# Kernel optimization log

Hardware: AMD Instinct MI355X
Metric: run time of the kernel (lower is better)

## Reference

```python
import jax, jax.numpy as jnp
import numpy as np

N_NODES = 50000

def setup_inputs() -> dict:
    key = jax.random.key(0)
    ks = jax.random.split(key, 8)
    d_in, d_h = 128, 128
    x = jax.random.normal(ks[0], (N_NODES, d_in), dtype=jnp.float32)
    edge_index = jax.random.randint(ks[1], (2, 800000), 0, N_NODES, dtype=jnp.int64)
    edge_pairs = jax.random.randint(ks[2], (1000000, 2), 0, N_NODES, dtype=jnp.int64)
    W_gcn = jax.random.normal(ks[3], (d_in, d_h), dtype=jnp.float32) / np.sqrt(d_in)
    b_gcn = jnp.zeros((d_h,), dtype=jnp.float32)
    W1 = jax.random.normal(ks[4], (2 * d_h, d_h), dtype=jnp.float32) / np.sqrt(2 * d_h)
    b1 = jnp.zeros((d_h,), dtype=jnp.float32)
    W2 = jax.random.normal(ks[5], (d_h, 1), dtype=jnp.float32) / np.sqrt(d_h)
    b2 = jnp.zeros((1,), dtype=jnp.float32)
    return {"x": x, "edge_index": edge_index, "edge_pairs": edge_pairs,
            "W_gcn": W_gcn, "b_gcn": b_gcn, "W1": W1, "b1": b1, "W2": W2, "b2": b2}

def gcn_conv(x, edge_index, W, b):
    # PyG GCNConv default: add self-loops, symmetric normalization.
    n = x.shape[0]
    loop = jnp.arange(n, dtype=edge_index.dtype)
    src = jnp.concatenate([edge_index[0], loop])  # [E+N]
    dst = jnp.concatenate([edge_index[1], loop])
    deg = jax.ops.segment_sum(jnp.ones(src.shape[0], dtype=x.dtype), dst, num_segments=n)
    dinv = jnp.where(deg > 0, jax.lax.rsqrt(deg), 0.0)
    norm = dinv[src] * dinv[dst]                  # [E+N]
    h = x @ W                                     # [N, H]
    agg = jax.ops.segment_sum(h[src] * norm[:, None], dst, num_segments=n)
    return agg + b

def reference(x, edge_index, edge_pairs, W_gcn, b_gcn, W1, b1, W2, b2):
    h = gcn_conv(x, edge_index, W_gcn, b_gcn)      # [N, H]
    e = jnp.concatenate([h[edge_pairs[:, 0]], h[edge_pairs[:, 1]]], axis=-1)  # [P, 2H]
    edge_logits = jax.nn.relu(e @ W1 + b1) @ W2 + b2  # [P, 1]
    return edge_logits, edge_pairs, h
```

## Files before the change

kernel.cpp:

```cpp
#include <hip/hip_runtime.h>
#include <hip/hip_fp16.h>

#define WG 256

typedef _Float16 f16;
typedef _Float16 hv2 __attribute__((ext_vector_type(2)));
typedef _Float16 f16x4 __attribute__((ext_vector_type(4)));
typedef _Float16 f16x8 __attribute__((ext_vector_type(8)));
typedef float f32x4 __attribute__((ext_vector_type(4)));

__global__ __launch_bounds__(WG) void k_count2(const int* __restrict__ dst,
                                               int* __restrict__ deg,
                                               int* __restrict__ rank,
                                               const int* __restrict__ pairs,
                                               int* __restrict__ pdeg,
                                               int* __restrict__ prank,
                                               int e, int p) {
    int i = blockIdx.x * WG + threadIdx.x;
    if (i < e) {
        rank[i] = atomicAdd(&deg[dst[i]], 1);
    } else if (i < e + p) {
        int j = i - e;
        prank[j] = atomicAdd(&pdeg[pairs[2 * j]], 1);
    }
}

__global__ __launch_bounds__(WG) void k_scan1x2(const int* __restrict__ deg,
                                                float* __restrict__ dinv,
                                                int* __restrict__ base,
                                                int* __restrict__ bsum,
                                                const int* __restrict__ pdeg,
                                                int* __restrict__ pbase,
                                                int* __restrict__ pbsum,
                                                int n, int nb) {
    __shared__ int t[WG];
    int tid = threadIdx.x;
    bool second = (blockIdx.x >= (unsigned)nb);
    int bid = second ? (blockIdx.x - nb) : blockIdx.x;
    const int* src = second ? pdeg : deg;
    int* dstb = second ? pbase : base;
    int* bs = second ? pbsum : bsum;
    int i = bid * WG + tid;
    int v = (i < n) ? src[i] : 0;
    if (!second && i < n) dinv[i] = rsqrtf((float)(v + 1));
    t[tid] = v;
    __syncthreads();
    for (int o = 1; o < WG; o <<= 1) {
        int add = (tid >= o) ? t[tid - o] : 0;
        __syncthreads();
        t[tid] += add;
        __syncthreads();
    }
    if (i < n) dstb[i] = t[tid] - v;
    if (tid == WG - 1) bs[bid] = t[WG - 1];
}

__global__ __launch_bounds__(WG) void k_scan23x2(int* __restrict__ base,
                                                 const int* __restrict__ bsum,
                                                 int* __restrict__ pbase,
                                                 const int* __restrict__ pbsum,
                                                 int n, int e, int p, int nb) {
    __shared__ int t[WG];
    int tid = threadIdx.x;
    bool second = (blockIdx.x >= (unsigned)nb);
    int bid = second ? (blockIdx.x - nb) : blockIdx.x;
    const int* bs = second ? pbsum : bsum;
    int* dstb = second ? pbase : base;
    int total = second ? p : e;
    int v = (tid < nb) ? bs[tid] : 0;
    t[tid] = v;
    __syncthreads();
    for (int o = 1; o < WG; o <<= 1) {
        int add = (tid >= o) ? t[tid - o] : 0;
        __syncthreads();
        t[tid] += add;
        __syncthreads();
    }
    int off = t[bid] - ((bid < nb) ? bs[bid] : 0);
    int i = bid * WG + tid;
    if (i < n) {
        dstb[i] += off;
        if (i == n - 1) dstb[n] = total;
    }
}

__global__ __launch_bounds__(WG) void k_fill2(const int* __restrict__ src,
                                              const int* __restrict__ dst,
                                              const int* __restrict__ base,
                                              const int* __restrict__ rank,
                                              int* __restrict__ esrc,
                                              const int* __restrict__ pairs,
                                              const int* __restrict__ pbase,
                                              const int* __restrict__ prank,
                                              int2* __restrict__ plist,
                                              int e, int p) {
    int i = blockIdx.x * WG + threadIdx.x;
    if (i < e) {
        esrc[base[dst[i]] + rank[i]] = src[i];
    } else if (i < e + p) {
        int j = i - e;
        int a = pairs[2 * j], b = pairs[2 * j + 1];
        plist[pbase[a] + prank[j]] = make_int2(b, j);
    }
}

__global__ __launch_bounds__(WG) void k_misc(const float* __restrict__ Wg,
                                             f16* __restrict__ Wgt,
                                             const float* __restrict__ W1,
                                             f16* __restrict__ W1t,
                                             const int* __restrict__ pairs,
                                             float* __restrict__ outp, int n4) {
    int b = blockIdx.x;
    if (b < 64) {
        int i = b * WG + threadIdx.x;
        int k = i & 127, nI = i >> 7;
        Wgt[i] = (f16)Wg[(size_t)k * 128 + nI];
    } else if (b < 192) {
        int i = (b - 64) * WG + threadIdx.x;
        int k = i & 255, nI = i >> 8;
        W1t[i] = (f16)W1[(size_t)k * 128 + nI];
    } else {
        int i = (b - 192) * WG + threadIdx.x;
        if (i < n4) {
            int4 v = ((const int4*)pairs)[i];
            ((float4*)outp)[i] = make_float4((float)v.x, (float)v.y, (float)v.z, (float)v.w);
        }
    }
}

__global__ __launch_bounds__(WG) void k_mm_hpk(const float* __restrict__ A,
                                               const f16* __restrict__ Wt,
                                               const float* __restrict__ dinv,
                                               __half2* __restrict__ Out, int n) {
    __shared__ f16 As[64][136];
    __shared__ f16 Bs[128][136];
    const int tid = threadIdx.x;
    const int row0 = blockIdx.x * 64;
    for (int f = tid; f < 128 * 16; f += WG) {
        int r = f >> 4, c = f & 15;
        *(float4*)&Bs[r][c * 8] = ((const float4*)Wt)[r * 16 + c];
    }
    for (int f = tid; f < 64 * 32; f += WG) {
        int r = f >> 5, c = f & 31;
        float4 v = make_float4(0.f, 0.f, 0.f, 0.f);
        if (row0 + r < n) v = ((const float4*)A)[(size_t)(row0 + r) * 32 + c];
        *(f16x4*)&As[r][c * 4] = (f16x4){(f16)v.x, (f16)v.y, (f16)v.z, (f16)v.w};
    }
    __syncthreads();
    const int wv = tid >> 6, lane = tid & 63, m = lane & 15, quad = lane >> 4;
    f32x4 acc[8];
#pragma unroll
    for (int t = 0; t < 8; ++t) acc[t] = (f32x4){0.f, 0.f, 0.f, 0.f};
#pragma unroll
    for (int kk = 0; kk < 4; ++kk) {
        f16x8 af = *(f16x8*)&As[wv * 16 + m][kk * 32 + quad * 8];
#pragma unroll
        for (int t = 0; t < 8; ++t) {
            f16x8 bf = *(f16x8*)&Bs[t * 16 + m][kk * 32 + quad * 8];
            acc[t] = __builtin_amdgcn_mfma_f32_16x16x32_f16(af, bf, acc[t], 0, 0, 0);
        }
    }
#pragma unroll
    for (int r = 0; r < 4; ++r) {
        int row = row0 + wv * 16 + quad * 4 + r;
        if (row < n) {
            float dv = dinv[row];
#pragma unroll
            for (int t = 0; t < 4; ++t)
                Out[(size_t)row * 64 + t * 16 + m] =
                    __floats2half2_rn(acc[t][r] * dv, acc[t + 4][r] * dv);
        }
    }
}

__global__ __launch_bounds__(WG) void k_mm_uv(const float* __restrict__ A,
                                              const f16* __restrict__ W1t,
                                              const float* __restrict__ b1,
                                              __half2* __restrict__ Up,
                                              __half2* __restrict__ Vp, int n) {
    __shared__ f16 As[64][136];
    __shared__ f16 Bs[128][136];
    const int tid = threadIdx.x;
    const int row0 = blockIdx.x * 64;
    for (int f = tid; f < 64 * 32; f += WG) {
        int r = f >> 5, c = f & 31;
        float4 v = make_float4(0.f, 0.f, 0.f, 0.f);
        if (row0 + r < n) v = ((const float4*)A)[(size_t)(row0 + r) * 32 + c];
        *(f16x4*)&As[r][c * 4] = (f16x4){(f16)v.x, (f16)v.y, (f16)v.z, (f16)v.w};
    }
    const int wv = tid >> 6, lane = tid & 63, m = lane & 15, quad = lane >> 4;
    f32x4 acc[8];
#pragma unroll
    for (int ph = 0; ph < 2; ++ph) {
        if (ph) __syncthreads();
        for (int f = tid; f < 128 * 16; f += WG) {
            int r = f >> 4, c = f & 15;
            *(float4*)&Bs[r][c * 8] = *(const float4*)(W1t + (size_t)r * 256 + ph * 128 + c * 8);
        }
        __syncthreads();
#pragma unroll
        for (int t = 0; t < 8; ++t) acc[t] = (f32x4){0.f, 0.f, 0.f, 0.f};
#pragma unroll
        for (int kk = 0; kk < 4; ++kk) {
            f16x8 af = *(f16x8*)&As[wv * 16 + m][kk * 32 + quad * 8];
#pragma unroll
            for (int t = 0; t < 8; ++t) {
                f16x8 bf = *(f16x8*)&Bs[t * 16 + m][kk * 32 + quad * 8];
                acc[t] = __builtin_amdgcn_mfma_f32_16x16x32_f16(af, bf, acc[t], 0, 0, 0);
            }
        }
        __half2* Out = ph ? Vp : Up;
#pragma unroll
        for (int t = 0; t < 4; ++t) {
            float bl = 0.f, bh = 0.f;
            if (!ph) { bl = b1[t * 16 + m]; bh = b1[t * 16 + m + 64]; }
#pragma unroll
            for (int r = 0; r < 4; ++r) {
                int row = row0 + wv * 16 + quad * 4 + r;
                if (row < n)
                    Out[(size_t)row * 64 + t * 16 + m] =
                        __floats2half2_rn(acc[t][r] + bl, acc[t + 4][r] + bh);
            }
        }
    }
}

__global__ __launch_bounds__(WG) void k_gather(const __half2* __restrict__ Hpk,
                                               const float* __restrict__ dinv,
                                               const float* __restrict__ bg,
                                               const int* __restrict__ base,
                                               const int* __restrict__ esrc,
                                               float* __restrict__ outh, int n) {
    int tid = threadIdx.x;
    int node = blockIdx.x * 16 + (tid >> 4);
    int sub = tid & 15;
    if (node >= n) return;
    int4 hh = *(const int4*)(Hpk + (size_t)node * 64 + 4 * sub);
    const int* hp = (const int*)&hh;
    float accl[4], acch[4];
#pragma unroll
    for (int k = 0; k < 4; ++k) {
        hv2 h = __builtin_bit_cast(hv2, hp[k]);
        accl[k] = (float)h[0];
        acch[k] = (float)h[1];
    }
    int j = base[node], jend = base[node + 1];
    for (; j + 4 <= jend; j += 4) {
        int s0 = esrc[j], s1 = esrc[j + 1], s2i = esrc[j + 2], s3 = esrc[j + 3];
        int4 r0 = *(const int4*)(Hpk + (size_t)s0 * 64 + 4 * sub);
        int4 r1 = *(const int4*)(Hpk + (size_t)s1 * 64 + 4 * sub);
        int4 r2 = *(const int4*)(Hpk + (size_t)s2i * 64 + 4 * sub);
        int4 r3 = *(const int4*)(Hpk + (size_t)s3 * 64 + 4 * sub);
        const int* p0 = (const int*)&r0;
        const int* p1 = (const int*)&r1;
        const int* p2 = (const int*)&r2;
        const int* p3 = (const int*)&r3;
#pragma unroll
        for (int k = 0; k < 4; ++k) {
            hv2 h0 = __builtin_bit_cast(hv2, p0[k]);
            hv2 h1 = __builtin_bit_cast(hv2, p1[k]);
            hv2 h2 = __builtin_bit_cast(hv2, p2[k]);
            hv2 h3 = __builtin_bit_cast(hv2, p3[k]);
            accl[k] += (float)h0[0] + (float)h1[0] + (float)h2[0] + (float)h3[0];
            acch[k] += (float)h0[1] + (float)h1[1] + (float)h2[1] + (float)h3[1];
        }
    }
    for (; j < jend; ++j) {
        int s = esrc[j];
        int4 r = *(const int4*)(Hpk + (size_t)s * 64 + 4 * sub);
        const int* pr = (const int*)&r;
#pragma unroll
        for (int k = 0; k < 4; ++k) {
            hv2 h = __builtin_bit_cast(hv2, pr[k]);
            accl[k] += (float)h[0];
            acch[k] += (float)h[1];
        }
    }
    float dv = dinv[node];
    float4 blo = *(const float4*)(bg + 4 * sub);
    float4 bhi = *(const float4*)(bg + 4 * sub + 64);
    *(float4*)&outh[(size_t)node * 128 + 4 * sub] =
        make_float4(fmaf(accl[0], dv, blo.x), fmaf(accl[1], dv, blo.y),
                    fmaf(accl[2], dv, blo.z), fmaf(accl[3], dv, blo.w));
    *(float4*)&outh[(size_t)node * 128 + 64 + 4 * sub] =
        make_float4(fmaf(acch[0], dv, bhi.x), fmaf(acch[1], dv, bhi.y),
                    fmaf(acch[2], dv, bhi.z), fmaf(acch[3], dv, bhi.w));
}

__global__ __launch_bounds__(WG) void k_pairs_csr(const __half2* __restrict__ U,
                                                  const __half2* __restrict__ V,
                                                  const float* __restrict__ W2,
                                                  const float* __restrict__ b2,
                                                  const int* __restrict__ pbase,
                                                  const int2* __restrict__ plist,
                                                  float* __restrict__ out_logit, int n) {
    int tid = threadIdx.x;
    int node = blockIdx.x * 16 + (tid >> 4);
    int sub = tid & 15;
    if (node >= n) return;
    int j = pbase[node], jend = pbase[node + 1];
    if (j >= jend) return;

    int4 uu = *(const int4*)(U + (size_t)node * 64 + 4 * sub);
    const int* ui = (const int*)&uu;

    float4 w2lo = ((const float4*)W2)[sub];
    float4 w2hi = ((const float4*)(W2 + 64))[sub];
    hv2 w2h[4];
    w2h[0] = hv2{(f16)w2lo.x, (f16)w2hi.x};
    w2h[1] = hv2{(f16)w2lo.y, (f16)w2hi.y};
    w2h[2] = hv2{(f16)w2lo.z, (f16)w2hi.z};
    w2h[3] = hv2{(f16)w2lo.w, (f16)w2hi.w};
    float bb = b2[0];
    const hv2 z2 = hv2{(f16)0.f, (f16)0.f};

    for (; j + 4 <= jend; j += 4) {
        int2 e0 = plist[j], e1 = plist[j + 1], e2 = plist[j + 2], e3 = plist[j + 3];
        int4 v0 = *(const int4*)(V + (size_t)e0.x * 64 + 4 * sub);
        int4 v1 = *(const int4*)(V + (size_t)e1.x * 64 + 4 * sub);
        int4 v2 = *(const int4*)(V + (size_t)e2.x * 64 + 4 * sub);
        int4 v3 = *(const int4*)(V + (size_t)e3.x * 64 + 4 * sub);
        const int* vi0 = (const int*)&v0;
        const int* vi1 = (const int*)&v1;
        const int* vi2 = (const int*)&v2;
        const int* vi3 = (const int*)&v3;
        float p0 = 0.f, p1 = 0.f, p2 = 0.f, p3 = 0.f;
#pragma unroll
        for (int k = 0; k < 4; ++k) {
            hv2 uk = __builtin_bit_cast(hv2, ui[k]);
            hv2 s0 = uk + __builtin_bit_cast(hv2, vi0[k]);
            hv2 s1 = uk + __builtin_bit_cast(hv2, vi1[k]);
            hv2 s2 = uk + __builtin_bit_cast(hv2, vi2[k]);
            hv2 s3 = uk + __builtin_bit_cast(hv2, vi3[k]);
            p0 = __builtin_amdgcn_fdot2(__builtin_elementwise_max(s0, z2), w2h[k], p0, false);
            p1 = __builtin_amdgcn_fdot2(__builtin_elementwise_max(s1, z2), w2h[k], p1, false);
            p2 = __builtin_amdgcn_fdot2(__builtin_elementwise_max(s2, z2), w2h[k], p2, false);
            p3 = __builtin_amdgcn_fdot2(__builtin_elementwise_max(s3, z2), w2h[k], p3, false);
        }
#pragma unroll
        for (int m = 1; m < 16; m <<= 1) {
            p0 += __shfl_xor(p0, m, 64);
            p1 += __shfl_xor(p1, m, 64);
            p2 += __shfl_xor(p2, m, 64);
            p3 += __shfl_xor(p3, m, 64);
        }
        if (sub == 0) {
            out_logit[e0.y] = p0 + bb;
            out_logit[e1.y] = p1 + bb;
            out_logit[e2.y] = p2 + bb;
            out_logit[e3.y] = p3 + bb;
        }
    }
    for (; j < jend; ++j) {
        int2 e0 = plist[j];
        int4 v0 = *(const int4*)(V + (size_t)e0.x * 64 + 4 * sub);
        const int* vi0 = (const int*)&v0;
        float p0 = 0.f;
#pragma unroll
        for (int k = 0; k < 4; ++k) {
            hv2 s0 = __builtin_bit_cast(hv2, ui[k]) + __builtin_bit_cast(hv2, vi0[k]);
            p0 = __builtin_amdgcn_fdot2(__builtin_elementwise_max(s0, z2), w2h[k], p0, false);
        }
#pragma unroll
        for (int m = 1; m < 16; m <<= 1) p0 += __shfl_xor(p0, m, 64);
        if (sub == 0) out_logit[e0.y] = p0 + bb;
    }
}

extern "C" void kernel_launch(void* const* d_in, const int* in_sizes, int n_in,
                              void* d_out, int out_size, void* d_ws, size_t ws_size,
                              hipStream_t stream) {
    const float* x     = (const float*)d_in[0];
    const int*   eidx  = (const int*)d_in[1];
    const int*   pairs = (const int*)d_in[2];
    const float* W_gcn = (const float*)d_in[3];
    const float* b_gcn = (const float*)d_in[4];
    const float* W1    = (const float*)d_in[5];
    const float* b1    = (const float*)d_in[6];
    const float* W2    = (const float*)d_in[7];
    const float* b2    = (const float*)d_in[8];

    const int N = in_sizes[0] / 128;
    const int E = in_sizes[1] / 2;
    const int P = in_sizes[2] / 2;
    const int* esrc_in = eidx;
    const int* edst_in = eidx + E;

    float* ws      = (float*)d_ws;
    int*   deg     = (int*)d_ws;
    int*   pdeg    = (int*)d_ws + N;
    float* dinv    = ws + 131072;
    int*   base    = (int*)(ws + 196608);
    int*   pbase   = (int*)(ws + 262144);
    int*   bsum    = (int*)(ws + 327680);
    int*   pbsum   = (int*)(ws + 327936);
    f16*   Wt_gcn  = (f16*)(ws + 328192);
    f16*   W1t     = (f16*)(ws + 336384);
    int*   rank    = (int*)(ws + 352768);
    int*   ecsr    = rank + (size_t)E;
    __half2* Hpk   = (__half2*)(ecsr + (size_t)E);
    int*   prank   = (int*)Hpk;
    __half2* Upk   = Hpk + (size_t)N * 64;
    __half2* Vpk   = Upk + (size_t)N * 64;
    int2*  plist   = (int2*)(Vpk + (size_t)N * 64);

    float* out_logit = (float*)d_out;
    float* out_pairs = out_logit + P;
    float* out_h     = out_logit + 3 * (size_t)P;

    const int nb = (N + WG - 1) / WG;
    dim3 blk(WG);
    dim3 grid_cnt((unsigned)((E + P + WG - 1) / WG));
    dim3 grid_misc((unsigned)(192 + (P / 2 + WG - 1) / WG));
    hipMemsetAsync(deg, 0, (size_t)(2 * N) * 4, stream);
    k_count2    <<<grid_cnt, blk, 0, stream>>>(edst_in, deg, rank, pairs, pdeg, prank, E, P);
    k_scan1x2   <<<2 * nb, blk, 0, stream>>>(deg, dinv, base, bsum, pdeg, pbase, pbsum, N, nb);
    k_scan23x2  <<<2 * nb, blk, 0, stream>>>(base, bsum, pbase, pbsum, N, E, P, nb);
    k_fill2     <<<grid_cnt, blk, 0, stream>>>(esrc_in, edst_in, base, rank, ecsr,
                                               pairs, pbase, prank, plist, E, P);
    k_misc      <<<grid_misc, blk, 0, stream>>>(W_gcn, Wt_gcn, W1, W1t, pairs, out_pairs, P / 2);
    k_mm_hpk    <<<(N + 63) / 64, blk, 0, stream>>>(x, Wt_gcn, dinv, Hpk, N);
    k_gather    <<<(N + 15) / 16, blk, 0, stream>>>(Hpk, dinv, b_gcn, base, ecsr, out_h, N);
    k_mm_uv     <<<(N + 63) / 64, blk, 0, stream>>>(out_h, W1t, b1, Upk, Vpk, N);
    k_pairs_csr <<<(N + 15) / 16, blk, 0, stream>>>(Upk, Vpk, W2, b2, pbase, plist, out_logit, N);
}
```

Measured before the change: 317.2 us.

## Interleave independent CSR-build stages with matmul and gather via role-split kernels

Reorganises the launch schedule so that independent work shares a kernel through even/odd block roles. The first kernel pairs edge degree counting with weight conversion and pair copy. The next pairs the edge scan fixup with the first matmul, then gather with pair counting, then the pair scan fixup with the UV matmul. The pair-CSR construction is pushed later so it overlaps with GCN compute instead of running serially up front. The pair rank buffer is moved into the output logit region. This adds idle role blocks and larger shared-memory allocations for the scan-role blocks, which may reduce occupancy.

```diff
diff --git a/kernel.cpp b/kernel.cpp
--- a/kernel.cpp
+++ b/kernel.cpp
@@ -9,40 +9,50 @@
 typedef _Float16 f16x8 __attribute__((ext_vector_type(8)));
 typedef float f32x4 __attribute__((ext_vector_type(4)));
 
-__global__ __launch_bounds__(WG) void k_count2(const int* __restrict__ dst,
+__global__ __launch_bounds__(WG) void k_fusedA(const float* __restrict__ Wg,
+                                               f16* __restrict__ Wgt,
+                                               const float* __restrict__ W1,
+                                               f16* __restrict__ W1t,
+                                               const int* __restrict__ pairs,
+                                               float* __restrict__ outp, int n4,
+                                               const int* __restrict__ dst,
                                                int* __restrict__ deg,
-                                               int* __restrict__ rank,
-                                               const int* __restrict__ pairs,
-                                               int* __restrict__ pdeg,
-                                               int* __restrict__ prank,
-                                               int e, int p) {
-    int i = blockIdx.x * WG + threadIdx.x;
-    if (i < e) {
-        rank[i] = atomicAdd(&deg[dst[i]], 1);
-    } else if (i < e + p) {
-        int j = i - e;
-        prank[j] = atomicAdd(&pdeg[pairs[2 * j]], 1);
-    }
-}
-
-__global__ __launch_bounds__(WG) void k_scan1x2(const int* __restrict__ deg,
-                                                float* __restrict__ dinv,
-                                                int* __restrict__ base,
-                                                int* __restrict__ bsum,
-                                                const int* __restrict__ pdeg,
-                                                int* __restrict__ pbase,
-                                                int* __restrict__ pbsum,
-                                                int n, int nb) {
+                                               int* __restrict__ rank, int e,
+                                               int nmisc, int necnt) {
+    int b = blockIdx.x, role = b & 1, idx = b >> 1;
+    if (role == 1) {
+        if (idx >= necnt) return;
+        int i = idx * WG + threadIdx.x;
+        if (i < e) rank[i] = atomicAdd(&deg[dst[i]], 1);
+        return;
+    }
+    if (idx >= nmisc) return;
+    if (idx < 64) {
+        int i = idx * WG + threadIdx.x;
+        int k = i & 127, nI = i >> 7;
+        Wgt[i] = (f16)Wg[(size_t)k * 128 + nI];
+    } else if (idx < 192) {
+        int i = (idx - 64) * WG + threadIdx.x;
+        int k = i & 255, nI = i >> 8;
+        W1t[i] = (f16)W1[(size_t)k * 128 + nI];
+    } else {
+        int i = (idx - 192) * WG + threadIdx.x;
+        if (i < n4) {
+            int4 v = ((const int4*)pairs)[i];
+            ((float4*)outp)[i] = make_float4((float)v.x, (float)v.y, (float)v.z, (float)v.w);
+        }
+    }
+}
+
+__global__ __launch_bounds__(WG) void k_scan1(const int* __restrict__ deg,
+                                              float* __restrict__ dinv,
+                                              int* __restrict__ base,
+                                              int* __restrict__ bsum, int n) {
     __shared__ int t[WG];
     int tid = threadIdx.x;
-    bool second = (blockIdx.x >= (unsigned)nb);
-    int bid = second ? (blockIdx.x - nb) : blockIdx.x;
-    const int* src = second ? pdeg : deg;
-    int* dstb = second ? pbase : base;
-    int* bs = second ? pbsum : bsum;
-    int i = bid * WG + tid;
-    int v = (i < n) ? src[i] : 0;
-    if (!second && i < n) dinv[i] = rsqrtf((float)(v + 1));
+    int i = blockIdx.x * WG + tid;
+    int v = (i < n) ? deg[i] : 0;
+    if (dinv && i < n) dinv[i] = rsqrtf((float)(v + 1));
     t[tid] = v;
     __syncthreads();
     for (int o = 1; o < WG; o <<= 1) {
@@ -51,91 +61,44 @@
         t[tid] += add;
         __syncthreads();
     }
-    if (i < n) dstb[i] = t[tid] - v;
-    if (tid == WG - 1) bs[bid] = t[WG - 1];
-}
-
-__global__ __launch_bounds__(WG) void k_scan23x2(int* __restrict__ base,
-                                                 const int* __restrict__ bsum,
-                                                 int* __restrict__ pbase,
-                                                 const int* __restrict__ pbsum,
-                                                 int n, int e, int p, int nb) {
-    __shared__ int t[WG];
-    int tid = threadIdx.x;
-    bool second = (blockIdx.x >= (unsigned)nb);
-    int bid = second ? (blockIdx.x - nb) : blockIdx.x;
-    const int* bs = second ? pbsum : bsum;
-    int* dstb = second ? pbase : base;
-    int total = second ? p : e;
-    int v = (tid < nb) ? bs[tid] : 0;
-    t[tid] = v;
-    __syncthreads();
-    for (int o = 1; o < WG; o <<= 1) {
-        int add = (tid >= o) ? t[tid - o] : 0;
-        __syncthreads();
-        t[tid] += add;
-        __syncthreads();
-    }
-    int off = t[bid] - ((bid < nb) ? bs[bid] : 0);
-    int i = bid * WG + tid;
-    if (i < n) {
-        dstb[i] += off;
-        if (i == n - 1) dstb[n] = total;
-    }
-}
-
-__global__ __launch_bounds__(WG) void k_fill2(const int* __restrict__ src,
-                                              const int* __restrict__ dst,
-                                              const int* __restrict__ base,
-                                              const int* __restrict__ rank,
-                                              int* __restrict__ esrc,
-                                              const int* __restrict__ pairs,
-                                              const int* __restrict__ pbase,
-                                              const int* __restrict__ prank,
-                                              int2* __restrict__ plist,
-                                              int e, int p) {
-    int i = blockIdx.x * WG + threadIdx.x;
-    if (i < e) {
-        esrc[base[dst[i]] + rank[i]] = src[i];
-    } else if (i < e + p) {
-        int j = i - e;
-        int a = pairs[2 * j], b = pairs[2 * j + 1];
-        plist[pbase[a] + prank[j]] = make_int2(b, j);
-    }
-}
-
-__global__ __launch_bounds__(WG) void k_misc(const float* __restrict__ Wg,
-                                             f16* __restrict__ Wgt,
-                                             const float* __restrict__ W1,
-                                             f16* __restrict__ W1t,
-                                             const int* __restrict__ pairs,
-                                             float* __restrict__ outp, int n4) {
-    int b = blockIdx.x;
-    if (b < 64) {
-        int i = b * WG + threadIdx.x;
-        int k = i & 127, nI = i >> 7;
-        Wgt[i] = (f16)Wg[(size_t)k * 128 + nI];
-    } else if (b < 192) {
-        int i = (b - 64) * WG + threadIdx.x;
-        int k = i & 255, nI = i >> 8;
-        W1t[i] = (f16)W1[(size_t)k * 128 + nI];
-    } else {
-        int i = (b - 192) * WG + threadIdx.x;
-        if (i < n4) {
-            int4 v = ((const int4*)pairs)[i];
-            ((float4*)outp)[i] = make_float4((float)v.x, (float)v.y, (float)v.z, (float)v.w);
-        }
-    }
-}
-
-__global__ __launch_bounds__(WG) void k_mm_hpk(const float* __restrict__ A,
+    if (i < n) base[i] = t[tid] - v;
+    if (tid == WG - 1) bsum[blockIdx.x] = t[WG - 1];
+}
+
+__global__ __launch_bounds__(WG) void k_fusedB(int* __restrict__ base,
+                                               const int* __restrict__ bsum,
+                                               int n, int total, int nb,
+                                               const float* __restrict__ A,
                                                const f16* __restrict__ Wt,
                                                const float* __restrict__ dinv,
-                                               __half2* __restrict__ Out, int n) {
-    __shared__ f16 As[64][136];
-    __shared__ f16 Bs[128][136];
-    const int tid = threadIdx.x;
-    const int row0 = blockIdx.x * 64;
+                                               __half2* __restrict__ Out, int nmm) {
+    __shared__ __align__(16) char smem[64 * 136 * 2 + 128 * 136 * 2];
+    int b = blockIdx.x, role = b & 1, idx = b >> 1;
+    int tid = threadIdx.x;
+    if (role == 0) {
+        if (idx >= nb) return;
+        int* t = (int*)smem;
+        int v = (tid < nb) ? bsum[tid] : 0;
+        t[tid] = v;
+        __syncthreads();
+        for (int o = 1; o < WG; o <<= 1) {
+            int add = (tid >= o) ? t[tid - o] : 0;
+            __syncthreads();
+            t[tid] += add;
+            __syncthreads();
+        }
+        int off = t[idx] - ((idx < nb) ? bsum[idx] : 0);
+        int i = idx * WG + tid;
+        if (i < n) {
+            base[i] += off;
+            if (i == n - 1) base[n] = total;
+        }
+        return;
+    }
+    if (idx >= nmm) return;
+    f16(*As)[136] = (f16(*)[136])smem;
+    f16(*Bs)[136] = (f16(*)[136])(smem + 64 * 136 * 2);
+    const int row0 = idx * 64;
     for (int f = tid; f < 128 * 16; f += WG) {
         int r = f >> 4, c = f & 15;
         *(float4*)&Bs[r][c * 8] = ((const float4*)Wt)[r * 16 + c];
@@ -173,66 +136,36 @@
     }
 }
 
-__global__ __launch_bounds__(WG) void k_mm_uv(const float* __restrict__ A,
-                                              const f16* __restrict__ W1t,
-                                              const float* __restrict__ b1,
-                                              __half2* __restrict__ Up,
-                                              __half2* __restrict__ Vp, int n) {
-    __shared__ f16 As[64][136];
-    __shared__ f16 Bs[128][136];
-    const int tid = threadIdx.x;
-    const int row0 = blockIdx.x * 64;
-    for (int f = tid; f < 64 * 32; f += WG) {
-        int r = f >> 5, c = f & 31;
-        float4 v = make_float4(0.f, 0.f, 0.f, 0.f);
-        if (row0 + r < n) v = ((const float4*)A)[(size_t)(row0 + r) * 32 + c];
-        *(f16x4*)&As[r][c * 4] = (f16x4){(f16)v.x, (f16)v.y, (f16)v.z, (f16)v.w};
-    }
-    const int wv = tid >> 6, lane = tid & 63, m = lane & 15, quad = lane >> 4;
-    f32x4 acc[8];
-#pragma unroll
-    for (int ph = 0; ph < 2; ++ph) {
-        if (ph) __syncthreads();
-        for (int f = tid; f < 128 * 16; f += WG) {
-            int r = f >> 4, c = f & 15;
-            *(float4*)&Bs[r][c * 8] = *(const float4*)(W1t + (size_t)r * 256 + ph * 128 + c * 8);
-        }
-        __syncthreads();
-#pragma unroll
-        for (int t = 0; t < 8; ++t) acc[t] = (f32x4){0.f, 0.f, 0.f, 0.f};
-#pragma unroll
-        for (int kk = 0; kk < 4; ++kk) {
-            f16x8 af = *(f16x8*)&As[wv * 16 + m][kk * 32 + quad * 8];
-#pragma unroll
-            for (int t = 0; t < 8; ++t) {
-                f16x8 bf = *(f16x8*)&Bs[t * 16 + m][kk * 32 + quad * 8];
-                acc[t] = __builtin_amdgcn_mfma_f32_16x16x32_f16(af, bf, acc[t], 0, 0, 0);
-            }
-        }
-        __half2* Out = ph ? Vp : Up;
-#pragma unroll
-        for (int t = 0; t < 4; ++t) {
-            float bl = 0.f, bh = 0.f;
-            if (!ph) { bl = b1[t * 16 + m]; bh = b1[t * 16 + m + 64]; }
-#pragma unroll
-            for (int r = 0; r < 4; ++r) {
-                int row = row0 + wv * 16 + quad * 4 + r;
-                if (row < n)
-                    Out[(size_t)row * 64 + t * 16 + m] =
-                        __floats2half2_rn(acc[t][r] + bl, acc[t + 4][r] + bh);
-            }
-        }
-    }
-}
-
-__global__ __launch_bounds__(WG) void k_gather(const __half2* __restrict__ Hpk,
+__global__ __launch_bounds__(WG) void k_fill(const int* __restrict__ src,
+                                             const int* __restrict__ dst,
+                                             const int* __restrict__ base,
+                                             const int* __restrict__ rank,
+                                             int* __restrict__ esrc, int e) {
+    int i = blockIdx.x * WG + threadIdx.x;
+    if (i >= e) return;
+    esrc[base[dst[i]] + rank[i]] = src[i];
+}
+
+__global__ __launch_bounds__(WG) void k_fusedC(const __half2* __restrict__ Hpk,
                                                const float* __restrict__ dinv,
                                                const float* __restrict__ bg,
                                                const int* __restrict__ base,
                                                const int* __restrict__ esrc,
-                                               float* __restrict__ outh, int n) {
+                                               float* __restrict__ outh, int n,
+                                               const int* __restrict__ pairs,
+                                               int* __restrict__ pdeg,
+                                               int* __restrict__ prank, int p,
+                                               int ngath, int npcnt) {
     int tid = threadIdx.x;
-    int node = blockIdx.x * 16 + (tid >> 4);
+    int b = blockIdx.x, role = b & 1, idx = b >> 1;
+    if (role == 1) {
+        if (idx >= npcnt) return;
+        int i = idx * WG + tid;
+        if (i < p) prank[i] = atomicAdd(&pdeg[pairs[2 * i]], 1);
+        return;
+    }
+    if (idx >= ngath) return;
+    int node = idx * 16 + (tid >> 4);
     int sub = tid & 15;
     if (node >= n) return;
     int4 hh = *(const int4*)(Hpk + (size_t)node * 64 + 4 * sub);
@@ -285,6 +218,94 @@
     *(float4*)&outh[(size_t)node * 128 + 64 + 4 * sub] =
         make_float4(fmaf(acch[0], dv, bhi.x), fmaf(acch[1], dv, bhi.y),
                     fmaf(acch[2], dv, bhi.z), fmaf(acch[3], dv, bhi.w));
+}
+
+__global__ __launch_bounds__(WG) void k_fusedD(int* __restrict__ pbase,
+                                               const int* __restrict__ pbsum,
+                                               int n, int total, int nb,
+                                               const float* __restrict__ A,
+                                               const f16* __restrict__ W1t,
+                                               const float* __restrict__ b1,
+                                               __half2* __restrict__ Up,
+                                               __half2* __restrict__ Vp, int nmm) {
+    __shared__ __align__(16) char smem[64 * 136 * 2 + 128 * 136 * 2];
+    int b = blockIdx.x, role = b & 1, idx = b >> 1;
+    int tid = threadIdx.x;
+    if (role == 0) {
+        if (idx >= nb) return;
+        int* t = (int*)smem;
+        int v = (tid < nb) ? pbsum[tid] : 0;
+        t[tid] = v;
+        __syncthreads();
+        for (int o = 1; o < WG; o <<= 1) {
+            int add = (tid >= o) ? t[tid - o] : 0;
+            __syncthreads();
+            t[tid] += add;
+            __syncthreads();
+        }
+        int off = t[idx] - ((idx < nb) ? pbsum[idx] : 0);
+        int i = idx * WG + tid;
+        if (i < n) {
+            pbase[i] += off;
+            if (i == n - 1) pbase[n] = total;
+        }
+        return;
+    }
+    if (idx >= nmm) return;
+    f16(*As)[136] = (f16(*)[136])smem;
+    f16(*Bs)[136] = (f16(*)[136])(smem + 64 * 136 * 2);
+    const int row0 = idx * 64;
+    for (int f = tid; f < 64 * 32; f += WG) {
+        int r = f >> 5, c = f & 31;
+        float4 v = make_float4(0.f, 0.f, 0.f, 0.f);
+        if (row0 + r < n) v = ((const float4*)A)[(size_t)(row0 + r) * 32 + c];
+        *(f16x4*)&As[r][c * 4] = (f16x4){(f16)v.x, (f16)v.y, (f16)v.z, (f16)v.w};
+    }
+    const int wv = tid >> 6, lane = tid & 63, m = lane & 15, quad = lane >> 4;
+    f32x4 acc[8];
+#pragma unroll
+    for (int ph = 0; ph < 2; ++ph) {
+        if (ph) __syncthreads();
+        for (int f = tid; f < 128 * 16; f += WG) {
+            int r = f >> 4, c = f & 15;
+            *(float4*)&Bs[r][c * 8] = *(const float4*)(W1t + (size_t)r * 256 + ph * 128 + c * 8);
+        }
+        __syncthreads();
+#pragma unroll
+        for (int t = 0; t < 8; ++t) acc[t] = (f32x4){0.f, 0.f, 0.f, 0.f};
+#pragma unroll
+        for (int kk = 0; kk < 4; ++kk) {
+            f16x8 af = *(f16x8*)&As[wv * 16 + m][kk * 32 + quad * 8];
+#pragma unroll
+            for (int t = 0; t < 8; ++t) {
+                f16x8 bf = *(f16x8*)&Bs[t * 16 + m][kk * 32 + quad * 8];
+                acc[t] = __builtin_amdgcn_mfma_f32_16x16x32_f16(af, bf, acc[t], 0, 0, 0);
+            }
+        }
+        __half2* Out = ph ? Vp : Up;
+#pragma unroll
+        for (int t = 0; t < 4; ++t) {
+            float bl = 0.f, bh = 0.f;
+            if (!ph) { bl = b1[t * 16 + m]; bh = b1[t * 16 + m + 64]; }
+#pragma unroll
+            for (int r = 0; r < 4; ++r) {
+                int row = row0 + wv * 16 + quad * 4 + r;
+                if (row < n)
+                    Out[(size_t)row * 64 + t * 16 + m] =
+                        __floats2half2_rn(acc[t][r] + bl, acc[t + 4][r] + bh);
+            }
+        }
+    }
+}
+
+__global__ __launch_bounds__(WG) void k_pfill(const int* __restrict__ pairs,
+                                              const int* __restrict__ pbase,
+                                              const int* __restrict__ prank,
+                                              int2* __restrict__ plist, int p) {
+    int j = blockIdx.x * WG + threadIdx.x;
+    if (j >= p) return;
+    int a = pairs[2 * j], bb = pairs[2 * j + 1];
+    plist[pbase[a] + prank[j]] = make_int2(bb, j);
 }
 
 __global__ __launch_bounds__(WG) void k_pairs_csr(const __half2* __restrict__ U,
@@ -399,7 +420,6 @@
     int*   rank    = (int*)(ws + 352768);
     int*   ecsr    = rank + (size_t)E;
     __half2* Hpk   = (__half2*)(ecsr + (size_t)E);
-    int*   prank   = (int*)Hpk;
     __half2* Upk   = Hpk + (size_t)N * 64;
     __half2* Vpk   = Upk + (size_t)N * 64;
     int2*  plist   = (int2*)(Vpk + (size_t)N * 64);
@@ -407,20 +427,30 @@
     float* out_logit = (float*)d_out;
     float* out_pairs = out_logit + P;
     float* out_h     = out_logit + 3 * (size_t)P;
-
-    const int nb = (N + WG - 1) / WG;
+    int*   prank   = (int*)d_out;
+
+    const int nb    = (N + WG - 1) / WG;
+    const int nmm   = (N + 63) / 64;
+    const int ngath = (N + 15) / 16;
+    const int nmisc = 192 + (P / 2 + WG - 1) / WG;
+    const int necnt = (E + WG - 1) / WG;
+    const int npcnt = (P + WG - 1) / WG;
     dim3 blk(WG);
-    dim3 grid_cnt((unsigned)((E + P + WG - 1) / WG));
-    dim3 grid_misc((unsigned)(192 + (P / 2 + WG - 1) / WG));
+
     hipMemsetAsync(deg, 0, (size_t)(2 * N) * 4, stream);
-    k_count2    <<<grid_cnt, blk, 0, stream>>>(edst_in, deg, rank, pairs, pdeg, prank, E, P);
-    k_scan1x2   <<<2 * nb, blk, 0, stream>>>(deg, dinv, base, bsum, pdeg, pbase, pbsum, N, nb);
-    k_scan23x2  <<<2 * nb, blk, 0, stream>>>(base, bsum, pbase, pbsum, N, E, P, nb);
-    k_fill2     <<<grid_cnt, blk, 0, stream>>>(esrc_in, edst_in, base, rank, ecsr,
-                                               pairs, pbase, prank, plist, E, P);
-    k_misc      <<<grid_misc, blk, 0, stream>>>(W_gcn, Wt_gcn, W1, W1t, pairs, out_pairs, P / 2);
-    k_mm_hpk    <<<(N + 63) / 64, blk, 0, stream>>>(x, Wt_gcn, dinv, Hpk, N);
-    k_gather    <<<(N + 15) / 16, blk, 0, stream>>>(Hpk, dinv, b_gcn, base, ecsr, out_h, N);
-    k_mm_uv     <<<(N + 63) / 64, blk, 0, stream>>>(out_h, W1t, b1, Upk, Vpk, N);
-    k_pairs_csr <<<(N + 15) / 16, blk, 0, stream>>>(Upk, Vpk, W2, b2, pbase, plist, out_logit, N);
-}
+    k_fusedA <<<2 * (nmisc > necnt ? nmisc : necnt), blk, 0, stream>>>(
+        W_gcn, Wt_gcn, W1, W1t, pairs, out_pairs, P / 2,
+        edst_in, deg, rank, E, nmisc, necnt);
+    k_scan1  <<<nb, blk, 0, stream>>>(deg, dinv, base, bsum, N);
+    k_fusedB <<<2 * (nb > nmm ? nb : nmm), blk, 0, stream>>>(
+        base, bsum, N, E, nb, x, Wt_gcn, dinv, Hpk, nmm);
+    k_fill   <<<necnt, blk, 0, stream>>>(esrc_in, edst_in, base, rank, ecsr, E);
+    k_fusedC <<<2 * (ngath > npcnt ? ngath : npcnt), blk, 0, stream>>>(
+        Hpk, dinv, b_gcn, base, ecsr, out_h, N,
+        pairs, pdeg, prank, P, ngath, npcnt);
+    k_scan1  <<<nb, blk, 0, stream>>>(pdeg, nullptr, pbase, pbsum, N);
+    k_fusedD <<<2 * (nb > nmm ? nb : nmm), blk, 0, stream>>>(
+        pbase, pbsum, N, P, nb, out_h, W1t, b1, Upk, Vpk, nmm);
+    k_pfill  <<<npcnt, blk, 0, stream>>>(pairs, pbase, prank, plist, P);
+    k_pairs_csr <<<ngath, blk, 0, stream>>>(Upk, Vpk, W2, b2, pbase, plist, out_logit, N);
+}
```

Measured after the change: 322.2 us. About the same (+1.6%).
